# Kernel tuning notes

Measured on AMD Instinct MI355X. Metric: run time of the kernel, lower is better.

Reference implementation:

```python
import jax, jax.numpy as jnp
import numpy as np

CHANNEL = 8
K_DIM = 16
D = CHANNEL * K_DIM
ROUT_IT = 3
TAU = 1.0
EPS = 1e-12  # torch F.normalize default


def _normalize(v):
    # L2 normalize over last dim, matching torch.nn.functional.normalize
    nrm = jnp.sqrt(jnp.sum(v * v, axis=-1, keepdims=True))
    return v / jnp.maximum(nrm, EPS)


def setup_inputs() -> dict:
    key = jax.random.key(0)
    k1, k2, k3, k4 = jax.random.split(key, 4)
    n, m = 50000, 32
    in_dim = D  # in_caps * k_dim = 8*16
    x = jax.random.normal(k1, (n, in_dim), dtype=jnp.float32)
    stdv = 1.0 / np.sqrt(float(in_dim))
    W = jax.random.uniform(k2, (D, in_dim), dtype=jnp.float32, minval=-stdv, maxval=stdv)
    b = jax.random.uniform(k3, (D,), dtype=jnp.float32, minval=-stdv, maxval=stdv)
    neighbor_id = jax.random.randint(k4, (n * m,), 0, n + 1, dtype=jnp.int64)
    return {"x": x, "W": W, "b": b, "neighbor_id": neighbor_id}


def reference(x, W, b, neighbor_id):
    n = x.shape[0]
    m = neighbor_id.shape[0] // n
    # fc + relu
    x = jax.nn.relu(x @ W.T + b)
    # per-capsule normalize
    x = _normalize(x.reshape(n, CHANNEL, K_DIM)).reshape(n, D)
    # append zero row for padded neighbor ids, gather neighbors
    z = jnp.concatenate([x, jnp.zeros((1, D), dtype=x.dtype)], axis=0)
    neighbors = z[neighbor_id].reshape(n, m, CHANNEL, K_DIM)
    x_caps = x.reshape(n, CHANNEL, K_DIM)
    u = x_caps
    for it in range(ROUT_IT):
        # agreement logits per (node, neighbor, channel)
        p = jnp.einsum('nck,nmck->nmc', u, neighbors)
        p = jax.nn.softmax(p / TAU, axis=-1)  # softmax over channels
        u = jnp.einsum('nmc,nmck->nck', p, neighbors) + x_caps
        if it < ROUT_IT - 1:
            u = _normalize(u)
    return u.reshape(n, D)
```

## Files before the change

### kernel.cpp

```cpp
#include <hip/hip_runtime.h>
#include <math.h>

#define CHANNEL 8
#define KDIM 16
#define DFULL 128
#define MNBR 32
#define ROUT_IT 3
#define TM1 64

typedef __attribute__((ext_vector_type(4))) float f32x4;
typedef __attribute__((ext_vector_type(8))) short short8;
typedef __attribute__((ext_vector_type(8))) _Float16 half8;
typedef __attribute__((ext_vector_type(2))) _Float16 half2v;

__device__ inline unsigned pk16(float a, float b) {
  auto r = __builtin_amdgcn_cvt_pkrtz(a, b);
  return __builtin_bit_cast(unsigned, r);
}
__device__ inline float fdot2(unsigned a, unsigned b, float c) {
  return __builtin_amdgcn_fdot2(__builtin_bit_cast(half2v, a),
                                __builtin_bit_cast(half2v, b), c, false);
}
__device__ inline float h2f_lo(unsigned w) {
  union { ushort u; _Float16 h; } v; v.u = (ushort)(w & 0xffffu); return (float)v.h;
}
__device__ inline float h2f_hi(unsigned w) {
  union { ushort u; _Float16 h; } v; v.u = (ushort)(w >> 16); return (float)v.h;
}
__device__ inline half2v h2(unsigned u) { return __builtin_bit_cast(half2v, u); }
__device__ inline unsigned unh(half2v h) { return __builtin_bit_cast(unsigned, h); }
__device__ inline unsigned pkfma16(unsigned a, unsigned b, unsigned c) {
  return unh(__builtin_elementwise_fma(h2(a), h2(b), h2(c)));
}
template <int C>
__device__ inline float dppadd(float x) {
  int m = __builtin_amdgcn_update_dpp(0, __builtin_bit_cast(int, x), C, 0xF, 0xF, true);
  return x + __builtin_bit_cast(float, m);
}

union H8 { unsigned u[4]; short8 v; };
__device__ inline short8 pack8h(float4 a, float4 b) {
  H8 r;
  r.u[0] = pk16(a.x, a.y); r.u[1] = pk16(a.z, a.w);
  r.u[2] = pk16(b.x, b.y); r.u[3] = pk16(b.z, b.w);
  return r.v;
}

__global__ __launch_bounds__(256) void wpack_kernel(const float* __restrict__ W,
                                                    ushort* __restrict__ wpk) {
  int task = blockIdx.x * 256 + threadIdx.x;
  if (task >= 2048) return;
  int f = task >> 6, l = task & 63;
  int kk = f >> 3, j = f & 7, L = l & 15, H = l >> 4;
  const float* src = W + (size_t)(j * 16 + L) * 128 + kk * 32 + H * 8;
  float4 a = *(const float4*)src;
  float4 b = *(const float4*)(src + 4);
  *(short8*)(wpk + (size_t)task * 8) = pack8h(a, b);
}

__global__ __launch_bounds__(256) void fc_mfma_kernel(
    const float* __restrict__ x, const ushort* __restrict__ wpk,
    const float* __restrict__ bias, ushort* __restrict__ z16, int n) {
  __shared__ __align__(16) float smem[TM1 * 132];

  const int t = threadIdx.x, lane = t & 63, w = t >> 6;

  {
    const uint4* gw = (const uint4*)wpk;
    uint4* lw = (uint4*)smem;
#pragma unroll
    for (int i = 0; i < 8; ++i) lw[i * 256 + t] = gw[i * 256 + t];
  }

  const int L = lane & 15, H = lane >> 4;
  const int r0 = blockIdx.x * TM1;
  const int row = r0 + w * 16 + L;
  const bool ok = row < n;
  const float4 z4 = make_float4(0.f, 0.f, 0.f, 0.f);

  const float* xr = x + (size_t)row * DFULL + H * 8;
  short8 af[4];
#pragma unroll
  for (int kk = 0; kk < 4; ++kk) {
    float4 xa = ok ? *(const float4*)(xr + kk * 32) : z4;
    float4 xb = ok ? *(const float4*)(xr + kk * 32 + 4) : z4;
    af[kk] = pack8h(xa, xb);
  }

  f32x4 acc[8];
#pragma unroll
  for (int j = 0; j < 8; ++j) {
    float bv = bias[j * 16 + L];
    acc[j] = (f32x4){bv, bv, bv, bv};
  }
  __syncthreads();
  const short8* wf = (const short8*)smem;
#pragma unroll
  for (int j = 0; j < 8; ++j)
#pragma unroll
    for (int kk = 0; kk < 4; ++kk) {
      short8 bfr = wf[(kk * 8 + j) * 64 + lane];
      acc[j] = __builtin_amdgcn_mfma_f32_16x16x32_f16(
          __builtin_bit_cast(half8, af[kk]), __builtin_bit_cast(half8, bfr),
          acc[j], 0, 0, 0);
    }
  __syncthreads();

  float* ys = smem;
  const int lr = w * 16 + H * 4;
#pragma unroll
  for (int j = 0; j < 8; ++j)
#pragma unroll
    for (int r = 0; r < 4; ++r)
      ys[(lr + r) * 132 + j * 16 + L] = fmaxf(acc[j][r], 0.f);
  __syncthreads();

#pragma unroll
  for (int pass = 0; pass < 2; ++pass) {
    int task = t + pass * 256;
    int rr = task >> 3, cc = task & 7;
    const float4* yr = (const float4*)(ys + rr * 132 + cc * 16);
    float4 a = yr[0], b = yr[1], c4 = yr[2], d4 = yr[3];
    float ss = a.x * a.x;
    ss = fmaf(a.y, a.y, ss); ss = fmaf(a.z, a.z, ss); ss = fmaf(a.w, a.w, ss);
    ss = fmaf(b.x, b.x, ss); ss = fmaf(b.y, b.y, ss); ss = fmaf(b.z, b.z, ss);
    ss = fmaf(b.w, b.w, ss); ss = fmaf(c4.x, c4.x, ss); ss = fmaf(c4.y, c4.y, ss);
    ss = fmaf(c4.z, c4.z, ss); ss = fmaf(c4.w, c4.w, ss); ss = fmaf(d4.x, d4.x, ss);
    ss = fmaf(d4.y, d4.y, ss); ss = fmaf(d4.z, d4.z, ss); ss = fmaf(d4.w, d4.w, ss);
    float sc = 1.f / fmaxf(sqrtf(ss), 1e-12f);
    int grow = r0 + rr;
    if (grow < n) {
      uint4 o0, o1;
      o0.x = pk16(a.x * sc, a.y * sc);  o0.y = pk16(a.z * sc, a.w * sc);
      o0.z = pk16(b.x * sc, b.y * sc);  o0.w = pk16(b.z * sc, b.w * sc);
      o1.x = pk16(c4.x * sc, c4.y * sc); o1.y = pk16(c4.z * sc, c4.w * sc);
      o1.z = pk16(d4.x * sc, d4.y * sc); o1.w = pk16(d4.z * sc, d4.w * sc);
      uint4* dst = (uint4*)(z16 + (size_t)grow * DFULL + cc * 16);
      dst[0] = o0; dst[1] = o1;
    } else if (grow == n) {
      uint4 zz = {0u, 0u, 0u, 0u};
      uint4* dst = (uint4*)(z16 + (size_t)grow * DFULL + cc * 16);
      dst[0] = zz; dst[1] = zz;
    }
  }
}

__global__ __launch_bounds__(256, 6) void routing_kernel(
    const ushort* __restrict__ z16, const int* __restrict__ nid,
    float* __restrict__ out, int n) {
  const int t = threadIdx.x;
  const int node = blockIdx.x * 4 + (t >> 6);
  if (node >= n) return;
  const int lane = t & 63;
  const int q = lane >> 3, c = lane & 7;

  int4 ids = *(const int4*)(nid + node * MNBR + 4 * q);
  const uint4* g0 = (const uint4*)(z16 + (size_t)ids.x * DFULL + c * KDIM);
  const uint4* g1 = (const uint4*)(z16 + (size_t)ids.y * DFULL + c * KDIM);
  const uint4* g2 = (const uint4*)(z16 + (size_t)ids.z * DFULL + c * KDIM);
  const uint4* g3 = (const uint4*)(z16 + (size_t)ids.w * DFULL + c * KDIM);
  uint4 R0a = g0[0], R0b = g0[1];
  uint4 R1a = g1[0], R1b = g1[1];
  uint4 R2a = g2[0], R2b = g2[1];
  uint4 R3a = g3[0], R3b = g3[1];
  unsigned r0[8] = {R0a.x, R0a.y, R0a.z, R0a.w, R0b.x, R0b.y, R0b.z, R0b.w};
  unsigned r1[8] = {R1a.x, R1a.y, R1a.z, R1a.w, R1b.x, R1b.y, R1b.z, R1b.w};
  unsigned r2[8] = {R2a.x, R2a.y, R2a.z, R2a.w, R2b.x, R2b.y, R2b.z, R2b.w};
  unsigned r3[8] = {R3a.x, R3a.y, R3a.z, R3a.w, R3b.x, R3b.y, R3b.z, R3b.w};

  const uint4* xp = (const uint4*)(z16 + (size_t)node * DFULL + c * KDIM);
  uint4 X0 = xp[0], X1 = xp[1];
  const unsigned EIGHTH = 0x30003000u;
  unsigned upk[8], xk8[8];
  {
    unsigned xpk[8] = {X0.x, X0.y, X0.z, X0.w, X1.x, X1.y, X1.z, X1.w};
#pragma unroll
    for (int i = 0; i < 8; ++i) {
      upk[i] = xpk[i];
      xk8[i] = unh(h2(xpk[i]) * h2(EIGHTH));
    }
  }

#pragma unroll
  for (int it = 0; it < ROUT_IT; ++it) {
    float A0 = 0.f, A1 = 0.f, A2 = 0.f, A3 = 0.f;
#pragma unroll
    for (int i = 0; i < 8; ++i) {
      A0 = fdot2(r0[i], upk[i], A0);
      A1 = fdot2(r1[i], upk[i], A1);
      A2 = fdot2(r2[i], upk[i], A2);
      A3 = fdot2(r3[i], upk[i], A3);
    }
    float e0 = __expf(A0), e1 = __expf(A1), e2 = __expf(A2), e3 = __expf(A3);
    float D0 = dppadd<0x141>(dppadd<0x4E>(dppadd<0xB1>(e0)));
    float D1 = dppadd<0x141>(dppadd<0x4E>(dppadd<0xB1>(e1)));
    float D2 = dppadd<0x141>(dppadd<0x4E>(dppadd<0xB1>(e2)));
    float D3 = dppadd<0x141>(dppadd<0x4E>(dppadd<0xB1>(e3)));
    unsigned sp0, sp1, sp2, sp3;
    {
      float s0 = e0 * __builtin_amdgcn_rcpf(D0);
      float s1 = e1 * __builtin_amdgcn_rcpf(D1);
      float s2 = e2 * __builtin_amdgcn_rcpf(D2);
      float s3 = e3 * __builtin_amdgcn_rcpf(D3);
      sp0 = pk16(s0, s0); sp1 = pk16(s1, s1);
      sp2 = pk16(s2, s2); sp3 = pk16(s3, s3);
    }
    unsigned acc[8];
#pragma unroll
    for (int i = 0; i < 8; ++i) {
      unsigned a = pkfma16(r3[i], sp3, xk8[i]);
      a = pkfma16(r2[i], sp2, a);
      a = pkfma16(r1[i], sp1, a);
      acc[i] = pkfma16(r0[i], sp0, a);
    }
#pragma unroll
    for (int i = 0; i < 8; ++i) {
      int v = __builtin_amdgcn_ds_swizzle((int)acc[i], 0x201F);
      acc[i] = unh(h2(acc[i]) + h2((unsigned)v));
    }
#pragma unroll
    for (int i = 0; i < 8; ++i) {
      int v = __builtin_amdgcn_ds_swizzle((int)acc[i], 0x401F);
      acc[i] = unh(h2(acc[i]) + h2((unsigned)v));
    }
#pragma unroll
    for (int i = 0; i < 8; ++i) {
      int v = __shfl_xor((int)acc[i], 32);
      acc[i] = unh(h2(acc[i]) + h2((unsigned)v));
    }

    if (it == ROUT_IT - 1) {
      unsigned a0 = (q & 1) ? acc[1] : acc[0];
      unsigned a1 = (q & 1) ? acc[3] : acc[2];
      unsigned a2 = (q & 1) ? acc[5] : acc[4];
      unsigned a3 = (q & 1) ? acc[7] : acc[6];
      unsigned b0 = (q & 2) ? a1 : a0;
      unsigned b1 = (q & 2) ? a3 : a2;
      unsigned sel = (q & 4) ? b1 : b0;
      float2 st; st.x = h2f_lo(sel); st.y = h2f_hi(sel);
      *(float2*)(out + (size_t)node * DFULL + c * KDIM + 2 * q) = st;
    } else {
      float ss = 0.f;
#pragma unroll
      for (int i = 0; i < 8; ++i) ss = fdot2(acc[i], acc[i], ss);
      float sc = __builtin_amdgcn_rsqf(fmaxf(ss, 1e-24f));
      unsigned scp = pk16(sc, sc);
#pragma unroll
      for (int i = 0; i < 8; ++i) upk[i] = unh(h2(acc[i]) * h2(scp));
    }
  }
}

extern "C" void kernel_launch(void* const* d_in, const int* in_sizes, int n_in,
                              void* d_out, int out_size, void* d_ws, size_t ws_size,
                              hipStream_t stream) {
  const float* x = (const float*)d_in[0];
  const float* W = (const float*)d_in[1];
  const float* b = (const float*)d_in[2];
  const int* nid = (const int*)d_in[3];
  float* out = (float*)d_out;

  int n = in_sizes[0] / DFULL;
  int g1 = (n + 1 + TM1 - 1) / TM1;
  size_t zrows = (size_t)g1 * TM1;

  ushort* z16 = (ushort*)d_ws;
  ushort* wpk = (ushort*)d_ws + zrows * DFULL;

  wpack_kernel<<<8, 256, 0, stream>>>(W, wpk);
  fc_mfma_kernel<<<g1, 256, 0, stream>>>(x, wpk, b, z16, n);
  routing_kernel<<<(n + 3) / 4, 256, 0, stream>>>(z16, nid, out, n);
}
```

Measured before the change: 146.7 us.

## Fuse weight packing into fc kernel and fold normalization into softmax exponent

Drops the separate weight-packing kernel, so each fc block converts W from fp32 to fp16 fragments directly into shared memory. This removes one launch and a round trip through the workspace, but every block now redoes the conversion. The routing kernel computes gather addresses with 32-bit byte offsets instead of 64-bit pointer math. It also skips the packed-half rescale of u after normalization and folds the scale and log2(e) into an exp2 argument. Because the unnormalized u is used in the weighted sum, the next iteration must still produce an equivalent result.

```diff
diff --git a/kernel.cpp b/kernel.cpp
--- a/kernel.cpp
+++ b/kernel.cpp
@@ -46,30 +46,25 @@
   return r.v;
 }
 
-__global__ __launch_bounds__(256) void wpack_kernel(const float* __restrict__ W,
-                                                    ushort* __restrict__ wpk) {
-  int task = blockIdx.x * 256 + threadIdx.x;
-  if (task >= 2048) return;
-  int f = task >> 6, l = task & 63;
-  int kk = f >> 3, j = f & 7, L = l & 15, H = l >> 4;
-  const float* src = W + (size_t)(j * 16 + L) * 128 + kk * 32 + H * 8;
-  float4 a = *(const float4*)src;
-  float4 b = *(const float4*)(src + 4);
-  *(short8*)(wpk + (size_t)task * 8) = pack8h(a, b);
-}
-
 __global__ __launch_bounds__(256) void fc_mfma_kernel(
-    const float* __restrict__ x, const ushort* __restrict__ wpk,
+    const float* __restrict__ x, const float* __restrict__ W,
     const float* __restrict__ bias, ushort* __restrict__ z16, int n) {
   __shared__ __align__(16) float smem[TM1 * 132];
 
   const int t = threadIdx.x, lane = t & 63, w = t >> 6;
 
   {
-    const uint4* gw = (const uint4*)wpk;
-    uint4* lw = (uint4*)smem;
-#pragma unroll
-    for (int i = 0; i < 8; ++i) lw[i * 256 + t] = gw[i * 256 + t];
+    short8* lw = (short8*)smem;
+#pragma unroll
+    for (int i = 0; i < 8; ++i) {
+      int task = t + i * 256;
+      int f = task >> 6, l = task & 63;
+      int kk = f >> 3, j = f & 7, L = l & 15, H = l >> 4;
+      const float* src = W + (size_t)(j * 16 + L) * 128 + kk * 32 + H * 8;
+      float4 a = *(const float4*)src;
+      float4 b = *(const float4*)(src + 4);
+      lw[task] = pack8h(a, b);
+    }
   }
 
   const int L = lane & 15, H = lane >> 4;
@@ -155,21 +150,23 @@
   const int q = lane >> 3, c = lane & 7;
 
   int4 ids = *(const int4*)(nid + node * MNBR + 4 * q);
-  const uint4* g0 = (const uint4*)(z16 + (size_t)ids.x * DFULL + c * KDIM);
-  const uint4* g1 = (const uint4*)(z16 + (size_t)ids.y * DFULL + c * KDIM);
-  const uint4* g2 = (const uint4*)(z16 + (size_t)ids.z * DFULL + c * KDIM);
-  const uint4* g3 = (const uint4*)(z16 + (size_t)ids.w * DFULL + c * KDIM);
-  uint4 R0a = g0[0], R0b = g0[1];
-  uint4 R1a = g1[0], R1b = g1[1];
-  uint4 R2a = g2[0], R2b = g2[1];
-  uint4 R3a = g3[0], R3b = g3[1];
+  const char* zb = (const char*)z16;
+  const unsigned cb = (unsigned)c * 32u;
+  unsigned o0 = ((unsigned)ids.x << 8) + cb;
+  unsigned o1 = ((unsigned)ids.y << 8) + cb;
+  unsigned o2 = ((unsigned)ids.z << 8) + cb;
+  unsigned o3 = ((unsigned)ids.w << 8) + cb;
+  uint4 R0a = *(const uint4*)(zb + o0), R0b = *(const uint4*)(zb + o0 + 16);
+  uint4 R1a = *(const uint4*)(zb + o1), R1b = *(const uint4*)(zb + o1 + 16);
+  uint4 R2a = *(const uint4*)(zb + o2), R2b = *(const uint4*)(zb + o2 + 16);
+  uint4 R3a = *(const uint4*)(zb + o3), R3b = *(const uint4*)(zb + o3 + 16);
   unsigned r0[8] = {R0a.x, R0a.y, R0a.z, R0a.w, R0b.x, R0b.y, R0b.z, R0b.w};
   unsigned r1[8] = {R1a.x, R1a.y, R1a.z, R1a.w, R1b.x, R1b.y, R1b.z, R1b.w};
   unsigned r2[8] = {R2a.x, R2a.y, R2a.z, R2a.w, R2b.x, R2b.y, R2b.z, R2b.w};
   unsigned r3[8] = {R3a.x, R3a.y, R3a.z, R3a.w, R3b.x, R3b.y, R3b.z, R3b.w};
 
-  const uint4* xp = (const uint4*)(z16 + (size_t)node * DFULL + c * KDIM);
-  uint4 X0 = xp[0], X1 = xp[1];
+  unsigned ox = ((unsigned)node << 8) + cb;
+  uint4 X0 = *(const uint4*)(zb + ox), X1 = *(const uint4*)(zb + ox + 16);
   const unsigned EIGHTH = 0x30003000u;
   unsigned upk[8], xk8[8];
   {
@@ -180,6 +177,7 @@
       xk8[i] = unh(h2(xpk[i]) * h2(EIGHTH));
     }
   }
+  float sc2 = 1.442695041f;
 
 #pragma unroll
   for (int it = 0; it < ROUT_IT; ++it) {
@@ -191,7 +189,10 @@
       A2 = fdot2(r2[i], upk[i], A2);
       A3 = fdot2(r3[i], upk[i], A3);
     }
-    float e0 = __expf(A0), e1 = __expf(A1), e2 = __expf(A2), e3 = __expf(A3);
+    float e0 = __builtin_amdgcn_exp2f(A0 * sc2);
+    float e1 = __builtin_amdgcn_exp2f(A1 * sc2);
+    float e2 = __builtin_amdgcn_exp2f(A2 * sc2);
+    float e3 = __builtin_amdgcn_exp2f(A3 * sc2);
     float D0 = dppadd<0x141>(dppadd<0x4E>(dppadd<0xB1>(e0)));
     float D1 = dppadd<0x141>(dppadd<0x4E>(dppadd<0xB1>(e1)));
     float D2 = dppadd<0x141>(dppadd<0x4E>(dppadd<0xB1>(e2)));
@@ -242,11 +243,12 @@
     } else {
       float ss = 0.f;
 #pragma unroll
-      for (int i = 0; i < 8; ++i) ss = fdot2(acc[i], acc[i], ss);
+      for (int i = 0; i < 8; ++i) {
+        upk[i] = acc[i];
+        ss = fdot2(acc[i], acc[i], ss);
+      }
       float sc = __builtin_amdgcn_rsqf(fmaxf(ss, 1e-24f));
-      unsigned scp = pk16(sc, sc);
-#pragma unroll
-      for (int i = 0; i < 8; ++i) upk[i] = unh(h2(acc[i]) * h2(scp));
+      sc2 = sc * 1.442695041f;
     }
   }
 }
@@ -262,12 +264,9 @@
 
   int n = in_sizes[0] / DFULL;
   int g1 = (n + 1 + TM1 - 1) / TM1;
-  size_t zrows = (size_t)g1 * TM1;
 
   ushort* z16 = (ushort*)d_ws;
-  ushort* wpk = (ushort*)d_ws + zrows * DFULL;
-
-  wpack_kernel<<<8, 256, 0, stream>>>(W, wpk);
-  fc_mfma_kernel<<<g1, 256, 0, stream>>>(x, wpk, b, z16, n);
+
+  fc_mfma_kernel<<<g1, 256, 0, stream>>>(x, W, b, z16, n);
   routing_kernel<<<(n + 3) / 4, 256, 0, stream>>>(z16, nid, out, n);
 }
```

Result: no change. 147.4 us (+0.5%).
